# Optimization experiments

Measured on AMD Instinct MI355X. Metric: run time of the kernel, lower is better.

Reference implementation:

```python
import jax, jax.numpy as jnp
import numpy as np

B, F, Q, E = 256, 128, 4096, 128
TAU = 0.2
P_DROP = 0.5
NUM_SAMPLES = 128  # hardcoded in forward: compute_scores(..., num_samples=128)
NUM_POS = 1
EASY_UB = 0.5
HARD_LB = 0.5


def setup_inputs() -> dict:
    k = jax.random.key(0)
    ks = jax.random.split(k, 8)
    query = jax.random.normal(ks[0], (B, F), jnp.float32)
    key = jax.random.normal(ks[1], (B, F), jnp.float32)
    teacher = jax.random.normal(ks[2], (B, F), jnp.float32)
    negatives = jax.random.normal(ks[3], (F, Q), jnp.float32)
    # random_maskout masks: rand <= p -> zero out
    mask_t = jax.random.uniform(ks[4], (E, B, F)) <= P_DROP
    mask_n = jax.random.uniform(ks[5], (E, F, Q)) <= P_DROP
    # compute_scores sampling mask: rand <= num_samples/Q
    score_mask = jax.random.uniform(ks[6], (E, B, Q)) <= (NUM_SAMPLES / Q)
    # bootstrap over batch dim: for each (e,q) column, sample B row indices with replacement
    idx = jax.random.randint(ks[7], (E, Q, B), 0, B)
    boot = jnp.zeros((E, Q, B), bool).at[
        jnp.arange(E)[:, None, None], jnp.arange(Q)[None, :, None], idx
    ].set(True)
    boot_mask = jnp.transpose(boot, (0, 2, 1))  # (E,B,Q)
    return dict(query=query, key=key, teacher=teacher, negatives=negatives,
                mask_t=mask_t, mask_n=mask_n, score_mask=score_mask, boot_mask=boot_mask)


def _masked_softmax(x, mask, axis):
    # matches torch masked_fill(~mask, -inf) + softmax; masked entries -> 0 prob
    z = jnp.where(mask, x, -jnp.inf)
    m = jnp.max(z, axis=axis, keepdims=True)
    m = jnp.where(jnp.isfinite(m), m, 0.0)  # guard fully-masked slices
    e = jnp.where(mask, jnp.exp(z - m), 0.0)
    return e / jnp.maximum(e.sum(axis=axis, keepdims=True), 1e-30)


def _l2norm(x, axis):
    n = jnp.sqrt(jnp.sum(x * x, axis=axis, keepdims=True))
    return x / jnp.maximum(n, 1e-12)


def reference(query, key, teacher, negatives, mask_t, mask_n, score_mask, boot_mask):
    negatives = jax.lax.stop_gradient(negatives)  # negatives.detach().clone()
    logits_pos = jnp.sum(query * key, axis=1, keepdims=True)      # (B,1)
    logits_neg = query @ negatives                                 # (B,Q)
    logits = jnp.concatenate([logits_pos, logits_neg], axis=1) / TAU
    moco_loss = -jax.nn.log_softmax(logits, axis=1)[:, 0].mean()   # CE with target 0

    # ---- teacher similarities (torch.no_grad) ----
    t = _l2norm(jnp.where(mask_t, 0.0, teacher[None, :, :]), 2)    # (E,B,F)
    n = _l2norm(jnp.where(mask_n, 0.0, negatives[None, :, :]), 1)  # (E,F,Q)
    sim = jax.lax.stop_gradient(jnp.einsum('ebf,efq->ebq', t, n) / TAU)

    # ---- scores: masked softmax over Q, masked mean over E ----
    probs = _masked_softmax(sim, score_mask, axis=2)               # (E,B,Q)
    cnt_e = jnp.maximum(score_mask.sum(axis=0).astype(sim.dtype), 1.0)
    scores = probs.sum(axis=0) / cnt_e                             # (B,Q)

    # ---- uncertainty: masked entropy over batch dim ----
    p = _masked_softmax(sim, boot_mask, axis=1) + 1e-7             # (E,B,Q)
    ent = -(p * jnp.log(p))
    cnt_b = jnp.maximum(boot_mask.sum(axis=1).astype(sim.dtype), 1.0)  # (E,Q)
    uncertainty = (ent.sum(axis=1) / cnt_b).mean(axis=0, keepdims=True)  # (1,Q)

    log_sm_neg = jax.nn.log_softmax(logits[:, 1:], axis=1)         # (B,Q)

    def _pos_loss(pos_mask_row):
        pm = jnp.broadcast_to(pos_mask_row, (B, Q))
        s = jnp.where(pm, scores, -jnp.inf)
        _, idx = jax.lax.top_k(s, NUM_POS)                         # (B,k)
        loss = -jnp.take_along_axis(log_sm_neg, idx, axis=1).mean(axis=1).mean()
        mask = jnp.zeros((B, Q), bool).at[jnp.arange(B)[:, None], idx].set(True)
        return loss, mask

    ub = jnp.quantile(uncertainty, EASY_UB, axis=1)                # (1,)
    easy_loss, easy_mask = _pos_loss(uncertainty <= ub)
    lb = jnp.quantile(uncertainty, HARD_LB, axis=1)
    hard_loss, hard_mask = _pos_loss(uncertainty >= lb)

    return moco_loss, logits, easy_loss, easy_mask, hard_loss, hard_mask
```

## Files before the change

kernel.cpp:

```cpp
#include <hip/hip_runtime.h>
#include <cmath>

typedef unsigned char u8;
typedef unsigned short u16;
typedef unsigned int u32;
typedef __attribute__((ext_vector_type(8))) short s8v;
typedef __attribute__((ext_vector_type(4))) float f32x4;

#define B 256
#define F 128
#define Q 4096
#define E 128
#define QW 128
#define INV_TAU 5.0f
#define CAP 256

#define W_SCORES 0u
#define W_CNT    1048576u
#define W_UNC    2097152u
#define W_NLSE   2101248u
#define W_MOCO   2101504u
#define W_EASY   2101760u
#define W_HARD   2102016u
#define W_UB     2102272u
#define W_INVN   2102528u
#define W_AF     2626816u
#define W_PB     4723968u
#define W_PS     8918272u
#define W_PN     13112576u
#define W_CNTB   15209728u
#define W_ENT    15242496u

#define O_MOCO   0u
#define O_LOGITS 1u
#define O_ELOSS  1048833u
#define O_EMASK  1048834u
#define O_HLOSS  2097410u
#define O_HMASK  2097411u

static __device__ __forceinline__ u16 f2bf(float x) {
    unsigned int u = __builtin_bit_cast(unsigned int, x);
    unsigned int r = (u + 0x7FFFu + ((u >> 16) & 1u)) >> 16;
    return (u16)r;
}

__global__ void k_zero(float* __restrict__ p) {
    p[(size_t)blockIdx.x * 256 + threadIdx.x] = 0.f;
}
__global__ void k_zeroi(int* __restrict__ p) {
    p[(size_t)blockIdx.x * 256 + threadIdx.x] = 0;
}

__global__ void __launch_bounds__(256) k_pack(const u8* __restrict__ in,
                                              u32* __restrict__ out, int Rin) {
    __shared__ u32 lds[64 * 133];
    int t = threadIdx.x;
    int r0 = blockIdx.x * 64;
    int q0 = blockIdx.y * 512;
    int qw0 = q0 >> 5;
    #pragma unroll
    for (int i = 0; i < 8; i++) {
        int w = i * 256 + t;
        int row = w >> 5, c = w & 31;
        uint4 v = *(const uint4*)&in[(size_t)(r0 + row) * Q + q0 + c * 16];
        int base = row * 133 + c * 4;
        lds[base] = v.x; lds[base + 1] = v.y; lds[base + 2] = v.z; lds[base + 3] = v.w;
    }
    __syncthreads();
    int e = r0 / Rin, rr = r0 % Rin;
    #pragma unroll
    for (int k = 0; k < 4; k++) {
        int qw = (t >> 6) + k * 4;
        int r = t & 63;
        u32 w = 0;
        #pragma unroll
        for (int j = 0; j < 8; j++) {
            u32 u = lds[r * 133 + qw * 8 + j];
            w |= ((u & 1u) | ((u >> 7) & 2u) | ((u >> 14) & 4u) | ((u >> 21) & 8u)) << (j * 4);
        }
        out[((size_t)e * QW + qw0 + qw) * Rin + rr + r] = w;
    }
}

__global__ void k_afrag(const float* __restrict__ teacher, const u8* __restrict__ mask_t,
                        u16* __restrict__ af) {
    int eb = blockIdx.x;
    int e  = eb >> 8;
    int b  = eb & (B - 1);
    int f  = threadIdx.x;
    float v = mask_t[(size_t)eb * F + f] ? 0.f : teacher[b * F + f];
    float ss = v * v;
    #pragma unroll
    for (int o = 32; o > 0; o >>= 1) ss += __shfl_down(ss, o);
    __shared__ float s2[2];
    if ((threadIdx.x & 63) == 0) s2[threadIdx.x >> 6] = ss;
    __syncthreads();
    float d = fmaxf(sqrtf(s2[0] + s2[1]), 1e-12f);
    float t = v / d;
    int bg = b >> 4, m = b & 15;
    int kb = f >> 5, quad = (f >> 3) & 3, j = f & 7;
    int lane = quad * 16 + m;
    af[((((size_t)e * 16 + bg) * 4 + kb) * 64 + lane) * 8 + j] = f2bf(t);
}

__global__ void k_invn(const float* __restrict__ neg, const u8* __restrict__ mask_n,
                       float* __restrict__ invn) {
    int e = blockIdx.x;
    int q = blockIdx.y * 256 + threadIdx.x;
    float ss = 0.f;
    #pragma unroll 4
    for (int f = 0; f < F; f++) {
        float v = mask_n[((size_t)e * F + f) * Q + q] ? 0.f : neg[f * Q + q];
        ss += v * v;
    }
    invn[e * Q + q] = INV_TAU / fmaxf(sqrtf(ss), 1e-12f);
}

__global__ void __launch_bounds__(256) k_fused(
        const u16* __restrict__ af, const float* __restrict__ neg,
        const u32* __restrict__ pn, const float* __restrict__ invn,
        const u32* __restrict__ pb, const u32* __restrict__ ps,
        float* __restrict__ unc, uint2* __restrict__ ent_buf,
        int* __restrict__ cnt_buf, int e0) {
    __shared__ u16 bfrag[2][4][64 * 8];
    __shared__ __align__(16) u32 bword[256];
    __shared__ __align__(16) u32 sword[256];
    __shared__ int sbase[256];
    __shared__ float mstat[4][32], sstat[4][32], cstat[4][32], estat[4][32];
    __shared__ float carr[32];

    int qb = blockIdx.x;
    int el = blockIdx.y, e = e0 + el;
    int t = threadIdx.x;
    int q0 = qb * 32;

    bword[t] = pb[((size_t)e * QW + qb) * B + t];
    sword[t] = ps[((size_t)e * QW + qb) * B + t];

    #pragma unroll
    for (int s = 0; s < 2; s++) {
        int slot = t + 256 * s;
        int qg = slot >> 8;
        int r = slot & 255;
        int kb = r >> 6, lane2 = r & 63;
        int q = q0 + qg * 16 + (lane2 & 15);
        int fb = kb * 32 + (lane2 >> 4) * 8;
        float iv = invn[e * Q + q];
        u16 tmp[8];
        #pragma unroll
        for (int j = 0; j < 8; j++) {
            u32 bit = (pn[((size_t)e * QW + qb) * F + fb + j] >> (q & 31)) & 1u;
            float v = bit ? 0.f : neg[(size_t)(fb + j) * Q + q] * iv;
            tmp[j] = f2bf(v);
        }
        *(s8v*)&bfrag[qg][kb][lane2 * 8] = *(const s8v*)tmp;
    }
    __syncthreads();

    int wave = t >> 6, lane = t & 63;
    int colb = lane & 15, quad = lane >> 4;
    f32x4 acc[4][2];
    #pragma unroll
    for (int bgi = 0; bgi < 4; bgi++) {
        int bg = wave * 4 + bgi;
        s8v a[4];
        #pragma unroll
        for (int kb = 0; kb < 4; kb++)
            a[kb] = *(const s8v*)&af[((((size_t)e * 16 + bg) * 4 + kb) * 64 + lane) * 8];
        #pragma unroll
        for (int qg = 0; qg < 2; qg++) {
            f32x4 c4 = {0.f, 0.f, 0.f, 0.f};
            #pragma unroll
            for (int kb = 0; kb < 4; kb++) {
                s8v bv = *(const s8v*)&bfrag[qg][kb][lane * 8];
                c4 = __builtin_amdgcn_mfma_f32_16x16x32_bf16(a[kb], bv, c4, 0, 0, 0);
            }
            acc[bgi][qg] = c4;
        }
    }

    u32 bwr[4][4];
    #pragma unroll
    for (int bgi = 0; bgi < 4; bgi++) {
        int b0 = (wave * 4 + bgi) * 16 + quad * 4;
        uint4 v = *(const uint4*)&bword[b0];
        bwr[bgi][0] = v.x; bwr[bgi][1] = v.y; bwr[bgi][2] = v.z; bwr[bgi][3] = v.w;
    }

    float mloc[2] = {-INFINITY, -INFINITY};
    #pragma unroll
    for (int bgi = 0; bgi < 4; bgi++)
        #pragma unroll
        for (int r = 0; r < 4; r++)
            #pragma unroll
            for (int qg = 0; qg < 2; qg++)
                if ((bwr[bgi][r] >> (qg * 16 + colb)) & 1u)
                    mloc[qg] = fmaxf(mloc[qg], acc[bgi][qg][r]);
    #pragma unroll
    for (int qg = 0; qg < 2; qg++) {
        mloc[qg] = fmaxf(mloc[qg], __shfl_xor(mloc[qg], 16));
        mloc[qg] = fmaxf(mloc[qg], __shfl_xor(mloc[qg], 32));
    }
    if (quad == 0) { mstat[wave][colb] = mloc[0]; mstat[wave][16 + colb] = mloc[1]; }
    __syncthreads();
    float Mg[2];
    #pragma unroll
    for (int qg = 0; qg < 2; qg++) {
        int col = qg * 16 + colb;
        float M = fmaxf(fmaxf(mstat[0][col], mstat[1][col]),
                        fmaxf(mstat[2][col], mstat[3][col]));
        Mg[qg] = (M == -INFINITY) ? 0.f : M;
    }

    float sloc[2] = {0.f, 0.f}, cloc[2] = {0.f, 0.f};
    #pragma unroll
    for (int bgi = 0; bgi < 4; bgi++)
        #pragma unroll
        for (int r = 0; r < 4; r++)
            #pragma unroll
            for (int qg = 0; qg < 2; qg++)
                if ((bwr[bgi][r] >> (qg * 16 + colb)) & 1u) {
                    sloc[qg] += __expf(acc[bgi][qg][r] - Mg[qg]);
                    cloc[qg] += 1.f;
                }
    #pragma unroll
    for (int qg = 0; qg < 2; qg++) {
        sloc[qg] += __shfl_xor(sloc[qg], 16); sloc[qg] += __shfl_xor(sloc[qg], 32);
        cloc[qg] += __shfl_xor(cloc[qg], 16); cloc[qg] += __shfl_xor(cloc[qg], 32);
    }
    if (quad == 0) {
        sstat[wave][colb] = sloc[0]; sstat[wave][16 + colb] = sloc[1];
        cstat[wave][colb] = cloc[0]; cstat[wave][16 + colb] = cloc[1];
    }
    __syncthreads();
    float invS[2];
    #pragma unroll
    for (int qg = 0; qg < 2; qg++) {
        int col = qg * 16 + colb;
        float S = sstat[0][col] + sstat[1][col] + sstat[2][col] + sstat[3][col];
        invS[qg] = 1.f / fmaxf(S, 1e-30f);
        if (wave == 0 && quad == 0)
            carr[col] = cstat[0][col] + cstat[1][col] + cstat[2][col] + cstat[3][col];
    }

    const float P0 = 1e-7f;
    const float C0 = 1.61180954e-6f;
    float eloc[2] = {0.f, 0.f};
    #pragma unroll
    for (int bgi = 0; bgi < 4; bgi++)
        #pragma unroll
        for (int r = 0; r < 4; r++)
            #pragma unroll
            for (int qg = 0; qg < 2; qg++) {
                if ((bwr[bgi][r] >> (qg * 16 + colb)) & 1u) {
                    float p = __expf(acc[bgi][qg][r] - Mg[qg]) * invS[qg] + P0;
                    eloc[qg] -= p * __logf(p);
                } else {
                    eloc[qg] += C0;
                }
            }
    #pragma unroll
    for (int qg = 0; qg < 2; qg++) {
        eloc[qg] += __shfl_xor(eloc[qg], 16); eloc[qg] += __shfl_xor(eloc[qg], 32);
    }
    if (quad == 0) { estat[wave][colb] = eloc[0]; estat[wave][16 + colb] = eloc[1]; }

    {
        u32 sw = sword[t];
        int n = __popc(sw);
        int base = 0;
        if (n) base = atomicAdd(&cnt_buf[el * B + t], n);
        sbase[t] = base;
    }
    __syncthreads();

    if (t < 32) {
        float tot = estat[0][t] + estat[1][t] + estat[2][t] + estat[3][t];
        atomicAdd(&unc[q0 + t], tot / fmaxf(carr[t], 1.f));
    }

    #pragma unroll
    for (int bgi = 0; bgi < 4; bgi++) {
        int b0 = (wave * 4 + bgi) * 16 + quad * 4;
        uint4 sv = *(const uint4*)&sword[b0];
        u32 svr[4] = {sv.x, sv.y, sv.z, sv.w};
        #pragma unroll
        for (int r = 0; r < 4; r++)
            #pragma unroll
            for (int qg = 0; qg < 2; qg++) {
                int c = qg * 16 + colb;
                u32 w = svr[r];
                if ((w >> c) & 1u) {
                    int pos = sbase[b0 + r] + __popc(w & ((1u << c) - 1u));
                    if (pos < CAP) {
                        uint2 en;
                        en.x = (unsigned)(q0 + c);
                        en.y = __builtin_bit_cast(unsigned, acc[bgi][qg][r]);
                        ent_buf[((size_t)(el * B + b0 + r)) * CAP + pos] = en;
                    }
                }
            }
    }
}

__global__ void __launch_bounds__(256) k_scores(
        const uint2* __restrict__ ent_buf, const int* __restrict__ cnt_buf,
        float* __restrict__ sacc, float* __restrict__ cacc, int ecnt) {
    __shared__ float srow[Q];
    __shared__ float crow[Q];
    int b = blockIdx.x, t = threadIdx.x;
    #pragma unroll
    for (int j = 0; j < 16; j++) { srow[t + 256 * j] = 0.f; crow[t + 256 * j] = 0.f; }
    __syncthreads();
    int wave = t >> 6, lane = t & 63;
    for (int el = wave; el < ecnt; el += 4) {
        int c = cnt_buf[el * B + b];
        if (c > CAP) c = CAP;
        if (c == 0) continue;
        const uint2* p = ent_buf + (size_t)(el * B + b) * CAP;
        uint2 ev[4]; int ne = 0;
        float m = -INFINITY;
        for (int i = lane; i < c; i += 64) {
            ev[ne] = p[i];
            m = fmaxf(m, __builtin_bit_cast(float, ev[ne].y));
            ne++;
        }
        #pragma unroll
        for (int off = 32; off > 0; off >>= 1) m = fmaxf(m, __shfl_xor(m, off));
        float s = 0.f; float ex[4];
        for (int k = 0; k < ne; k++) {
            ex[k] = __expf(__builtin_bit_cast(float, ev[k].y) - m);
            s += ex[k];
        }
        #pragma unroll
        for (int off = 32; off > 0; off >>= 1) s += __shfl_xor(s, off);
        float iS = 1.f / fmaxf(s, 1e-30f);
        for (int k = 0; k < ne; k++) {
            atomicAdd(&srow[ev[k].x], ex[k] * iS);
            atomicAdd(&crow[ev[k].x], 1.f);
        }
    }
    __syncthreads();
    #pragma unroll
    for (int j = 0; j < 16; j++) {
        int q = t + 256 * j;
        sacc[(size_t)b * Q + q] += srow[q];
        cacc[(size_t)b * Q + q] += crow[q];
    }
}

__global__ void k_finscores(float* __restrict__ sacc, const float* __restrict__ cacc) {
    int idx = blockIdx.x * 256 + threadIdx.x;
    sacc[idx] = sacc[idx] / fmaxf(cacc[idx], 1.f);
}

__global__ void k_logits(const float* __restrict__ query, const float* __restrict__ key,
                         const float* __restrict__ neg, float* __restrict__ out) {
    __shared__ float qrow[F];
    __shared__ float red[256];
    int b = blockIdx.x, t = threadIdx.x;
    float pp = 0.f;
    if (t < F) { float qv = query[b * F + t]; qrow[t] = qv; pp = qv * key[b * F + t]; }
    red[t] = pp;
    __syncthreads();
    for (int s = 128; s > 0; s >>= 1) { if (t < s) red[t] += red[t + s]; __syncthreads(); }
    float pos = red[0];
    float acc[16];
    #pragma unroll
    for (int j = 0; j < 16; j++) acc[j] = 0.f;
    for (int f = 0; f < F; f++) {
        float a = qrow[f];
        const float* np_ = neg + (size_t)f * Q + t;
        #pragma unroll
        for (int j = 0; j < 16; j++) acc[j] = fmaf(a, np_[256 * j], acc[j]);
    }
    float* row = out + O_LOGITS + (size_t)b * (Q + 1);
    #pragma unroll
    for (int j = 0; j < 16; j++) row[1 + t + 256 * j] = acc[j] * INV_TAU;
    if (t == 0) row[0] = pos * INV_TAU;
}

__global__ void k_rowstats(const float* __restrict__ out, float* __restrict__ moco_part,
                           float* __restrict__ nlse) {
    __shared__ float red[256];
    int b = blockIdx.x, t = threadIdx.x;
    const float* row = out + O_LOGITS + (size_t)b * (Q + 1);
    float m = -INFINITY, mn = -INFINITY;
    for (int j = 0; j < 17; j++) {
        int i = t + 256 * j;
        if (i < Q + 1) { float zz = row[i]; m = fmaxf(m, zz); if (i >= 1) mn = fmaxf(mn, zz); }
    }
    red[t] = m; __syncthreads();
    for (int s = 128; s > 0; s >>= 1) { if (t < s) red[t] = fmaxf(red[t], red[t + s]); __syncthreads(); }
    float M = red[0]; __syncthreads();
    red[t] = mn; __syncthreads();
    for (int s = 128; s > 0; s >>= 1) { if (t < s) red[t] = fmaxf(red[t], red[t + s]); __syncthreads(); }
    float Mn = red[0]; __syncthreads();
    float s1 = 0.f, s2 = 0.f;
    for (int j = 0; j < 17; j++) {
        int i = t + 256 * j;
        if (i < Q + 1) { float zz = row[i]; s1 += expf(zz - M); if (i >= 1) s2 += expf(zz - Mn); }
    }
    red[t] = s1; __syncthreads();
    for (int s = 128; s > 0; s >>= 1) { if (t < s) red[t] += red[t + s]; __syncthreads(); }
    float S = red[0]; __syncthreads();
    red[t] = s2; __syncthreads();
    for (int s = 128; s > 0; s >>= 1) { if (t < s) red[t] += red[t + s]; __syncthreads(); }
    float Sn = red[0];
    if (t == 0) { moco_part[b] = M + logf(S) - row[0]; nlse[b] = Mn + logf(Sn); }
}

__global__ void k_median(float* __restrict__ unc, float* __restrict__ ubp) {
    __shared__ float sd[4096];
    int t = threadIdx.x;
    #pragma unroll
    for (int j = 0; j < 4; j++) {
        int q = t + 1024 * j;
        float u = unc[q] * (1.f / 128.f);
        unc[q] = u; sd[q] = u;
    }
    __syncthreads();
    for (int k = 2; k <= 4096; k <<= 1) {
        for (int j = k >> 1; j > 0; j >>= 1) {
            #pragma unroll
            for (int base = 0; base < 4; base++) {
                int i = t + 1024 * base;
                int ixj = i ^ j;
                if (ixj > i) {
                    bool up = ((i & k) == 0);
                    float x = sd[i], y = sd[ixj];
                    if ((x > y) == up) { sd[i] = y; sd[ixj] = x; }
                }
            }
            __syncthreads();
        }
    }
    if (t == 0) { float a = sd[2047], b2 = sd[2048]; ubp[0] = a + 0.5f * (b2 - a); }
}

__global__ void k_select(float* __restrict__ out, const float* __restrict__ scores,
                         const float* __restrict__ unc, const float* __restrict__ ubp,
                         const float* __restrict__ nlse, float* __restrict__ easy_part,
                         float* __restrict__ hard_part) {
    __shared__ float rv[256];
    __shared__ int ri[256];
    __shared__ int bshare;
    int b = blockIdx.x, mode = blockIdx.y, t = threadIdx.x;
    float ub = ubp[0];
    float bv = -INFINITY; int bidx = Q;
    #pragma unroll
    for (int j = 0; j < 16; j++) {
        int q = t + 256 * j;
        float u = unc[q];
        bool ok = (mode == 0) ? (u <= ub) : (u >= ub);
        if (ok) {
            float v = scores[(size_t)b * Q + q];
            if (v > bv || (v == bv && q < bidx)) { bv = v; bidx = q; }
        }
    }
    rv[t] = bv; ri[t] = bidx; __syncthreads();
    for (int s = 128; s > 0; s >>= 1) {
        if (t < s) {
            float v2 = rv[t + s]; int i2 = ri[t + s];
            if (v2 > rv[t] || (v2 == rv[t] && i2 < ri[t])) { rv[t] = v2; ri[t] = i2; }
        }
        __syncthreads();
    }
    if (t == 0) {
        int best = ri[0]; bshare = best;
        float zz = out[O_LOGITS + (size_t)b * (Q + 1) + 1 + best];
        float loss = nlse[b] - zz;
        (mode == 0 ? easy_part : hard_part)[b] = loss;
    }
    __syncthreads();
    int best = bshare;
    float* mrow = out + (mode == 0 ? O_EMASK : O_HMASK) + (size_t)b * Q;
    #pragma unroll
    for (int j = 0; j < 16; j++) { int q = t + 256 * j; mrow[q] = (q == best) ? 1.f : 0.f; }
}

__global__ void k_scalars(const float* __restrict__ moco, const float* __restrict__ easyp,
                          const float* __restrict__ hardp, float* __restrict__ out) {
    __shared__ float red[256];
    int t = threadIdx.x;
    red[t] = moco[t]; __syncthreads();
    for (int s = 128; s > 0; s >>= 1) { if (t < s) red[t] += red[t + s]; __syncthreads(); }
    if (t == 0) out[O_MOCO] = red[0] / 256.f;
    __syncthreads();
    red[t] = easyp[t]; __syncthreads();
    for (int s = 128; s > 0; s >>= 1) { if (t < s) red[t] += red[t + s]; __syncthreads(); }
    if (t == 0) out[O_ELOSS] = red[0] / 256.f;
    __syncthreads();
    red[t] = hardp[t]; __syncthreads();
    for (int s = 128; s > 0; s >>= 1) { if (t < s) red[t] += red[t + s]; __syncthreads(); }
    if (t == 0) out[O_HLOSS] = red[0] / 256.f;
}

extern "C" void kernel_launch(void* const* d_in, const int* in_sizes, int n_in,
                              void* d_out, int out_size, void* d_ws, size_t ws_size,
                              hipStream_t stream) {
    const float* query   = (const float*)d_in[0];
    const float* key     = (const float*)d_in[1];
    const float* teacher = (const float*)d_in[2];
    const float* neg     = (const float*)d_in[3];
    const u8* mask_t     = (const u8*)d_in[4];
    const u8* mask_n     = (const u8*)d_in[5];
    const u8* score_mask = (const u8*)d_in[6];
    const u8* boot_mask  = (const u8*)d_in[7];
    float* out = (float*)d_out;
    float* ws  = (float*)d_ws;

    long ws_floats = (long)(ws_size / 4);
    int Ec = (int)((ws_floats - (long)W_ENT) / (long)(B * CAP * 2));
    if (Ec > E) Ec = E;
    if (Ec < 1) Ec = 1;

    u16* af = (u16*)(ws + W_AF);
    u32* pb = (u32*)(ws + W_PB);
    u32* ps = (u32*)(ws + W_PS);
    u32* pn = (u32*)(ws + W_PN);
    int* cnt_buf = (int*)(ws + W_CNTB);
    uint2* ent_buf = (uint2*)(ws + W_ENT);

    k_zero<<<2101248 / 256, 256, 0, stream>>>(ws + W_SCORES);
    k_pack<<<dim3((E * B) / 64, Q / 512), 256, 0, stream>>>(boot_mask, pb, B);
    k_pack<<<dim3((E * B) / 64, Q / 512), 256, 0, stream>>>(score_mask, ps, B);
    k_pack<<<dim3((E * F) / 64, Q / 512), 256, 0, stream>>>(mask_n, pn, F);
    k_afrag<<<E * B, 128, 0, stream>>>(teacher, mask_t, af);
    k_invn<<<dim3(E, Q / 256), 256, 0, stream>>>(neg, mask_n, ws + W_INVN);
    k_logits<<<B, 256, 0, stream>>>(query, key, neg, out);
    k_rowstats<<<B, 256, 0, stream>>>(out, ws + W_MOCO, ws + W_NLSE);

    for (int e0 = 0; e0 < E; e0 += Ec) {
        int ecnt = (E - e0 < Ec) ? (E - e0) : Ec;
        k_zeroi<<<ecnt, 256, 0, stream>>>(cnt_buf);
        k_fused<<<dim3(QW, ecnt), 256, 0, stream>>>(
            af, neg, pn, ws + W_INVN, pb, ps, ws + W_UNC, ent_buf, cnt_buf, e0);
        k_scores<<<B, 256, 0, stream>>>(ent_buf, cnt_buf, ws + W_SCORES, ws + W_CNT, ecnt);
    }

    k_finscores<<<(B * Q) / 256, 256, 0, stream>>>(ws + W_SCORES, ws + W_CNT);
    k_median<<<1, 1024, 0, stream>>>(ws + W_UNC, ws + W_UB);
    k_select<<<dim3(B, 2), 256, 0, stream>>>(out, ws + W_SCORES, ws + W_UNC, ws + W_UB,
                                             ws + W_NLSE, ws + W_EASY, ws + W_HARD);
    k_scalars<<<1, 256, 0, stream>>>(ws + W_MOCO, ws + W_EASY, ws + W_HARD, out);
}
```

Baseline: 1.443 ms.

## Vectorize zero/logits loads, read packed mask in invn, cache softmax exps

```diff
diff --git a/kernel.cpp b/kernel.cpp
--- a/kernel.cpp
+++ b/kernel.cpp
@@ -44,8 +44,8 @@
     return (u16)r;
 }
 
-__global__ void k_zero(float* __restrict__ p) {
-    p[(size_t)blockIdx.x * 256 + threadIdx.x] = 0.f;
+__global__ void k_zero(float4* __restrict__ p) {
+    p[(size_t)blockIdx.x * 256 + threadIdx.x] = make_float4(0.f, 0.f, 0.f, 0.f);
 }
 __global__ void k_zeroi(int* __restrict__ p) {
     p[(size_t)blockIdx.x * 256 + threadIdx.x] = 0;
@@ -103,17 +103,35 @@
     af[((((size_t)e * 16 + bg) * 4 + kb) * 64 + lane) * 8 + j] = f2bf(t);
 }
 
-__global__ void k_invn(const float* __restrict__ neg, const u8* __restrict__ mask_n,
-                       float* __restrict__ invn) {
-    int e = blockIdx.x;
-    int q = blockIdx.y * 256 + threadIdx.x;
-    float ss = 0.f;
+__global__ void __launch_bounds__(256) k_invn(const float* __restrict__ neg,
+                                              const u32* __restrict__ pn,
+                                              float* __restrict__ invn) {
+    __shared__ u32 lds[32 * 128];
+    int e = blockIdx.x, t = threadIdx.x;
+    int qblk = blockIdx.y;
+    size_t base = ((size_t)e * QW + qblk * 32) * F;
+    #pragma unroll
+    for (int k = 0; k < 16; k++) lds[t + 256 * k] = pn[base + t + 256 * k];
+    __syncthreads();
+    int q0 = qblk * 1024 + t * 4;
+    int qwl = (t * 4) >> 5;
+    int sh = (t * 4) & 31;
+    float s0 = 0.f, s1 = 0.f, s2 = 0.f, s3 = 0.f;
     #pragma unroll 4
     for (int f = 0; f < F; f++) {
-        float v = mask_n[((size_t)e * F + f) * Q + q] ? 0.f : neg[f * Q + q];
-        ss += v * v;
-    }
-    invn[e * Q + q] = INV_TAU / fmaxf(sqrtf(ss), 1e-12f);
+        float4 v = *(const float4*)&neg[(size_t)f * Q + q0];
+        u32 w = lds[qwl * 128 + f] >> sh;
+        if (!(w & 1u)) s0 = fmaf(v.x, v.x, s0);
+        if (!(w & 2u)) s1 = fmaf(v.y, v.y, s1);
+        if (!(w & 4u)) s2 = fmaf(v.z, v.z, s2);
+        if (!(w & 8u)) s3 = fmaf(v.w, v.w, s3);
+    }
+    float4 r;
+    r.x = INV_TAU / fmaxf(sqrtf(s0), 1e-12f);
+    r.y = INV_TAU / fmaxf(sqrtf(s1), 1e-12f);
+    r.z = INV_TAU / fmaxf(sqrtf(s2), 1e-12f);
+    r.w = INV_TAU / fmaxf(sqrtf(s3), 1e-12f);
+    *(float4*)&invn[(size_t)e * Q + q0] = r;
 }
 
 __global__ void __launch_bounds__(256) k_fused(
@@ -212,17 +230,20 @@
         Mg[qg] = (M == -INFINITY) ? 0.f : M;
     }
 
+    float ex[4][2][4];
     float sloc[2] = {0.f, 0.f}, cloc[2] = {0.f, 0.f};
     #pragma unroll
     for (int bgi = 0; bgi < 4; bgi++)
         #pragma unroll
         for (int r = 0; r < 4; r++)
             #pragma unroll
-            for (int qg = 0; qg < 2; qg++)
-                if ((bwr[bgi][r] >> (qg * 16 + colb)) & 1u) {
-                    sloc[qg] += __expf(acc[bgi][qg][r] - Mg[qg]);
-                    cloc[qg] += 1.f;
-                }
+            for (int qg = 0; qg < 2; qg++) {
+                bool mk = (bwr[bgi][r] >> (qg * 16 + colb)) & 1u;
+                float v = mk ? __expf(acc[bgi][qg][r] - Mg[qg]) : 0.f;
+                ex[bgi][qg][r] = v;
+                sloc[qg] += v;
+                cloc[qg] += mk ? 1.f : 0.f;
+            }
     #pragma unroll
     for (int qg = 0; qg < 2; qg++) {
         sloc[qg] += __shfl_xor(sloc[qg], 16); sloc[qg] += __shfl_xor(sloc[qg], 32);
@@ -253,7 +274,7 @@
             #pragma unroll
             for (int qg = 0; qg < 2; qg++) {
                 if ((bwr[bgi][r] >> (qg * 16 + colb)) & 1u) {
-                    float p = __expf(acc[bgi][qg][r] - Mg[qg]) * invS[qg] + P0;
+                    float p = ex[bgi][qg][r] * invS[qg] + P0;
                     eloc[qg] -= p * __logf(p);
                 } else {
                     eloc[qg] += C0;
@@ -327,16 +348,16 @@
         }
         #pragma unroll
         for (int off = 32; off > 0; off >>= 1) m = fmaxf(m, __shfl_xor(m, off));
-        float s = 0.f; float ex[4];
+        float s = 0.f; float exv[4];
         for (int k = 0; k < ne; k++) {
-            ex[k] = __expf(__builtin_bit_cast(float, ev[k].y) - m);
-            s += ex[k];
+            exv[k] = __expf(__builtin_bit_cast(float, ev[k].y) - m);
+            s += exv[k];
         }
         #pragma unroll
         for (int off = 32; off > 0; off >>= 1) s += __shfl_xor(s, off);
         float iS = 1.f / fmaxf(s, 1e-30f);
         for (int k = 0; k < ne; k++) {
-            atomicAdd(&srow[ev[k].x], ex[k] * iS);
+            atomicAdd(&srow[ev[k].x], exv[k] * iS);
             atomicAdd(&crow[ev[k].x], 1.f);
         }
     }
@@ -365,18 +386,30 @@
     __syncthreads();
     for (int s = 128; s > 0; s >>= 1) { if (t < s) red[t] += red[t + s]; __syncthreads(); }
     float pos = red[0];
-    float acc[16];
-    #pragma unroll
-    for (int j = 0; j < 16; j++) acc[j] = 0.f;
+    float4 acc[4];
+    #pragma unroll
+    for (int j = 0; j < 4; j++) acc[j] = make_float4(0.f, 0.f, 0.f, 0.f);
     for (int f = 0; f < F; f++) {
         float a = qrow[f];
-        const float* np_ = neg + (size_t)f * Q + t;
-        #pragma unroll
-        for (int j = 0; j < 16; j++) acc[j] = fmaf(a, np_[256 * j], acc[j]);
+        const float* np_ = neg + (size_t)f * Q + t * 4;
+        #pragma unroll
+        for (int j = 0; j < 4; j++) {
+            float4 v = *(const float4*)&np_[1024 * j];
+            acc[j].x = fmaf(a, v.x, acc[j].x);
+            acc[j].y = fmaf(a, v.y, acc[j].y);
+            acc[j].z = fmaf(a, v.z, acc[j].z);
+            acc[j].w = fmaf(a, v.w, acc[j].w);
+        }
     }
     float* row = out + O_LOGITS + (size_t)b * (Q + 1);
     #pragma unroll
-    for (int j = 0; j < 16; j++) row[1 + t + 256 * j] = acc[j] * INV_TAU;
+    for (int j = 0; j < 4; j++) {
+        int q = t * 4 + 1024 * j;
+        row[1 + q]     = acc[j].x * INV_TAU;
+        row[1 + q + 1] = acc[j].y * INV_TAU;
+        row[1 + q + 2] = acc[j].z * INV_TAU;
+        row[1 + q + 3] = acc[j].w * INV_TAU;
+    }
     if (t == 0) row[0] = pos * INV_TAU;
 }
 
@@ -522,12 +555,12 @@
     int* cnt_buf = (int*)(ws + W_CNTB);
     uint2* ent_buf = (uint2*)(ws + W_ENT);
 
-    k_zero<<<2101248 / 256, 256, 0, stream>>>(ws + W_SCORES);
+    k_zero<<<2052, 256, 0, stream>>>((float4*)(ws + W_SCORES));
     k_pack<<<dim3((E * B) / 64, Q / 512), 256, 0, stream>>>(boot_mask, pb, B);
     k_pack<<<dim3((E * B) / 64, Q / 512), 256, 0, stream>>>(score_mask, ps, B);
     k_pack<<<dim3((E * F) / 64, Q / 512), 256, 0, stream>>>(mask_n, pn, F);
     k_afrag<<<E * B, 128, 0, stream>>>(teacher, mask_t, af);
-    k_invn<<<dim3(E, Q / 256), 256, 0, stream>>>(neg, mask_n, ws + W_INVN);
+    k_invn<<<dim3(E, 4), 256, 0, stream>>>(neg, pn, ws + W_INVN);
     k_logits<<<B, 256, 0, stream>>>(query, key, neg, out);
     k_rowstats<<<B, 256, 0, stream>>>(out, ws + W_MOCO, ws + W_NLSE);
 
```

New measurement: 1.429 ms. No clear change (-0.9%).
